# Performance work log

Hardware: AMD Instinct MI355X
Metric: run time of the kernel (lower is better)

## Reference

```python
import jax, jax.numpy as jnp
import numpy as np

D_MODEL = 1024
NUM_HEADS = 16
DEPTH = D_MODEL // NUM_HEADS  # 64
B, S = 4, 2048


def setup_inputs() -> dict:
    key = jax.random.key(0)
    ks = jax.random.split(key, 9)
    scale = 1.0 / np.sqrt(D_MODEL)
    inp = {
        "x": jax.random.normal(ks[0], (B, S, D_MODEL), dtype=jnp.float32),
        "Wq": jax.random.normal(ks[1], (D_MODEL, D_MODEL), dtype=jnp.float32) * scale,
        "bq": jnp.zeros((D_MODEL,), dtype=jnp.float32),
        "Wk": jax.random.normal(ks[2], (D_MODEL, D_MODEL), dtype=jnp.float32) * scale,
        "bk": jnp.zeros((D_MODEL,), dtype=jnp.float32),
        "Wv": jax.random.normal(ks[3], (D_MODEL, D_MODEL), dtype=jnp.float32) * scale,
        "bv": jnp.zeros((D_MODEL,), dtype=jnp.float32),
        "Wo": jax.random.normal(ks[4], (D_MODEL, D_MODEL), dtype=jnp.float32) * scale,
        "bo": jnpps if False else jnp.zeros((D_MODEL,), dtype=jnp.float32),
    }
    return inp


def reference(x, Wq, bq, Wk, bk, Wv, bv, Wo, bo):
    # q/k/v projections: [B, S, D]
    q = x @ Wq + bq
    k = x @ Wk + bk
    v = x @ Wv + bv

    def split_heads(t):  # [B, S, D] -> [B, H, S, depth]
        return t.reshape(B, S, NUM_HEADS, DEPTH).transpose(0, 2, 1, 3)

    q, k, v = split_heads(q), split_heads(k), split_heads(v)

    # scaled dot-product attention
    scores = jnp.einsum("bhqd,bhkd->bhqk", q, k) / jnp.sqrt(jnp.float32(DEPTH))
    attn = jax.nn.softmax(scores, axis=-1)  # [B, H, Sq, Sk]
    out = jnp.einsum("bhqk,bhkd->bhqd", attn, v)

    # merge heads: [B, H, S, depth] -> [B, S, D]
    out = out.transpose(0, 2, 1, 3).reshape(B, S, D_MODEL)
    return out @ Wo + bo
```

## Files before the change

kernel.cpp:

```cpp
#include <hip/hip_runtime.h>
#include <cstdint>

typedef __attribute__((ext_vector_type(8))) __bf16 bf16x8;
typedef __attribute__((ext_vector_type(4))) __bf16 bf16x4;
typedef __attribute__((ext_vector_type(4))) float f32x4;

#define S_LEN 2048
#define NH 16
#define DMODEL 1024
#define M_ROWS 8192

__device__ __forceinline__ void gload16(const void* g, void* l) {
  __builtin_amdgcn_global_load_lds(
      (const __attribute__((address_space(1))) void*)const_cast<void*>(g),
      (__attribute__((address_space(3))) void*)l, 16, 0, 0);
}

__global__ __launch_bounds__(256) void split_x_kernel(
    const float* __restrict__ in, __bf16* __restrict__ hi, __bf16* __restrict__ lo)
{
  const size_t i = ((size_t)blockIdx.x * 256 + threadIdx.x) * 4;
  const float4 v = *(const float4*)(in + i);
  const float vv[4] = {v.x, v.y, v.z, v.w};
  bf16x4 h, l;
#pragma unroll
  for (int j = 0; j < 4; ++j) {
    const __bf16 hb = (__bf16)vv[j];
    h[j] = hb;
    l[j] = (__bf16)(vv[j] - (float)hb);
  }
  *(bf16x4*)(hi + i) = h;
  *(bf16x4*)(lo + i) = l;
}

__global__ __launch_bounds__(256) void tsplit_w_kernel(
    const float* __restrict__ W, __bf16* __restrict__ th, __bf16* __restrict__ tl)
{
  __shared__ float tile[32][33];
  const int t = threadIdx.x;
  const int n0 = blockIdx.x * 32, k0 = blockIdx.y * 32;
  {
    const int r = t >> 3, c = (t & 7) * 4;
    const float4 v = *(const float4*)(W + (size_t)(k0 + r) * DMODEL + n0 + c);
    tile[r][c] = v.x; tile[r][c + 1] = v.y; tile[r][c + 2] = v.z; tile[r][c + 3] = v.w;
  }
  __syncthreads();
  const int n = t >> 3, kk = (t & 7) * 4;
  bf16x4 h, l;
#pragma unroll
  for (int j = 0; j < 4; ++j) {
    const float v = tile[kk + j][n];
    const __bf16 hb = (__bf16)v;
    h[j] = hb;
    l[j] = (__bf16)(v - (float)hb);
  }
  *(bf16x4*)(th + (size_t)(n0 + n) * DMODEL + k0 + kk) = h;
  *(bf16x4*)(tl + (size_t)(n0 + n) * DMODEL + k0 + kk) = l;
}

__global__ __launch_bounds__(256) void gemm_bf16x3_kernel(
    const __bf16* __restrict__ Ah, const __bf16* __restrict__ Al,
    const __bf16* __restrict__ Bh, const __bf16* __restrict__ Bl,
    const float* __restrict__ bias, float* __restrict__ outF,
    __bf16* __restrict__ outB, const int mode, const float scale)
{
  __shared__ __align__(16) __bf16 sAh[128 * 32];
  __shared__ __align__(16) __bf16 sAl[128 * 32];
  __shared__ __align__(16) __bf16 sBh[128 * 32];
  __shared__ __align__(16) __bf16 sBl[128 * 32];

  const int tid = threadIdx.x;
  const int w = tid >> 6, l = tid & 63;
  const int wr = w >> 1, wc = w & 1;
  const int m0 = blockIdx.x * 128, n0 = blockIdx.y * 128;
  const int q = l & 15, kg = l >> 4;

  f32x4 acc[4][4];
#pragma unroll
  for (int i = 0; i < 4; ++i)
#pragma unroll
    for (int j = 0; j < 4; ++j) acc[i][j] = f32x4{0.f, 0.f, 0.f, 0.f};

  const int sr0 = w * 32 + (l >> 2);
  const int sg = l & 3;

  for (int k0 = 0; k0 < 1024; k0 += 32) {
    __syncthreads();
#pragma unroll
    for (int u = 0; u < 2; ++u) {
      const int r = sr0 + u * 16;
      const int gs = sg ^ ((r >> 1) & 3);
      const size_t offA = (size_t)(m0 + r) * 1024 + k0 + gs * 8;
      const size_t offB = (size_t)(n0 + r) * 1024 + k0 + gs * 8;
      const int ldsoff = w * 2048 + u * 1024;
      gload16(Ah + offA, (char*)sAh + ldsoff);
      gload16(Al + offA, (char*)sAl + ldsoff);
      gload16(Bh + offB, (char*)sBh + ldsoff);
      gload16(Bl + offB, (char*)sBl + ldsoff);
    }
    __syncthreads();

    bf16x8 fah[4], fal[4], fbh[4], fbl[4];
#pragma unroll
    for (int mf = 0; mf < 4; ++mf) {
      const int row = wr * 64 + mf * 16 + q;
      const int off = row * 64 + ((kg ^ ((row >> 1) & 3)) * 16);
      fah[mf] = *(const bf16x8*)((const char*)sAh + off);
      fal[mf] = *(const bf16x8*)((const char*)sAl + off);
    }
#pragma unroll
    for (int nf = 0; nf < 4; ++nf) {
      const int n = wc * 64 + nf * 16 + q;
      const int off = n * 64 + ((kg ^ ((n >> 1) & 3)) * 16);
      fbh[nf] = *(const bf16x8*)((const char*)sBh + off);
      fbl[nf] = *(const bf16x8*)((const char*)sBl + off);
    }
#pragma unroll
    for (int mf = 0; mf < 4; ++mf)
#pragma unroll
      for (int nf = 0; nf < 4; ++nf) {
        acc[mf][nf] = __builtin_amdgcn_mfma_f32_16x16x32_bf16(fah[mf], fbh[nf], acc[mf][nf], 0, 0, 0);
        acc[mf][nf] = __builtin_amdgcn_mfma_f32_16x16x32_bf16(fah[mf], fbl[nf], acc[mf][nf], 0, 0, 0);
        acc[mf][nf] = __builtin_amdgcn_mfma_f32_16x16x32_bf16(fal[mf], fbh[nf], acc[mf][nf], 0, 0, 0);
      }
  }

#pragma unroll
  for (int mf = 0; mf < 4; ++mf) {
#pragma unroll
    for (int nf = 0; nf < 4; ++nf) {
      const int nloc = wc * 64 + nf * 16 + q;
      const int n = n0 + nloc;
      const float bv = bias[n];
      const int mbase = m0 + wr * 64 + mf * 16 + kg * 4;
      if (mode == 0) {
#pragma unroll
        for (int r = 0; r < 4; ++r)
          outF[(size_t)(mbase + r) * 1024 + n] = acc[mf][nf][r] + bv;
      } else if (mode == 1) {
#pragma unroll
        for (int r = 0; r < 4; ++r) {
          const int m = mbase + r;
          const int b = m >> 11, s = m & 2047, h = n >> 6, d = n & 63;
          outB[(((size_t)(b * NH + h)) * S_LEN + s) * 64 + d] =
              (__bf16)((acc[mf][nf][r] + bv) * scale);
        }
      } else {
        const int b = mbase >> 11, s0 = mbase & 2047, h = n >> 6, d = n & 63;
        bf16x4 pv;
#pragma unroll
        for (int r = 0; r < 4; ++r) pv[r] = (__bf16)(acc[mf][nf][r] + bv);
        *(bf16x4*)(outB + (((size_t)(b * NH + h)) * 64 + d) * S_LEN + s0) = pv;
      }
    }
  }
}

__global__ __launch_bounds__(256) void attn_mfma_kernel(
    const __bf16* __restrict__ qbuf, const __bf16* __restrict__ kbuf,
    const __bf16* __restrict__ vbufT, __bf16* __restrict__ o_hi,
    __bf16* __restrict__ o_lo)
{
  __shared__ __align__(16) __bf16 Ks[64 * 64];
  __shared__ __align__(16) __bf16 Vt[64 * 64];
  __shared__ __align__(16) __bf16 Pt[4 * 32 * 64];

  const int tid = threadIdx.x;
  const int w = tid >> 6, l = tid & 63;
  const int q = l & 15, kg = l >> 4;
  const int q7 = q & 7;
  const int bh = blockIdx.y;
  const int q0 = blockIdx.x * 128;

  bf16x8 qf[2][2];
#pragma unroll
  for (int qg = 0; qg < 2; ++qg) {
    const __bf16* qp =
        qbuf + ((size_t)bh * S_LEN + q0 + w * 32 + qg * 16 + q) * 64 + kg * 8;
    qf[qg][0] = *(const bf16x8*)qp;
    qf[qg][1] = *(const bf16x8*)(qp + 32);
  }

  float l_s[2] = {0.f, 0.f};
  f32x4 acc_o[2][4];
#pragma unroll
  for (int qg = 0; qg < 2; ++qg)
#pragma unroll
    for (int i = 0; i < 4; ++i) acc_o[qg][i] = f32x4{0.f, 0.f, 0.f, 0.f};

  char* const Pw = (char*)Pt + w * 4096;
  const int sr = w * 16 + (l >> 3);
  const int sg = l & 7;

  const int koff0 = q * 128 + ((kg ^ q7) << 4);
  const int koff1 = q * 128 + (((kg + 4) ^ q7) << 4);
  int voff[2];
#pragma unroll
  for (int kf = 0; kf < 2; ++kf) voff[kf] = ((kf * 4 + kg) ^ q7) << 4;

  for (int t = 0; t < S_LEN / 64; ++t) {
    __syncthreads();
#pragma unroll
    for (int u = 0; u < 2; ++u) {
      const int r = sr + u * 8;
      const int gs = sg ^ (r & 7);
      const int ldsoff = w * 2048 + u * 1024;
      gload16(kbuf + ((size_t)bh * S_LEN + t * 64 + r) * 64 + gs * 8, (char*)Ks + ldsoff);
      gload16(vbufT + ((size_t)bh * 64 + r) * S_LEN + t * 64 + gs * 8, (char*)Vt + ldsoff);
    }
    __syncthreads();

    f32x4 sacc[2][4];
#pragma unroll
    for (int qg = 0; qg < 2; ++qg)
#pragma unroll
      for (int mf = 0; mf < 4; ++mf) sacc[qg][mf] = f32x4{0.f, 0.f, 0.f, 0.f};

    __builtin_amdgcn_s_setprio(1);
#pragma unroll
    for (int mf = 0; mf < 4; ++mf) {
      const bf16x8 a0 = *(const bf16x8*)((const char*)Ks + mf * 2048 + koff0);
      const bf16x8 a1 = *(const bf16x8*)((const char*)Ks + mf * 2048 + koff1);
#pragma unroll
      for (int qg = 0; qg < 2; ++qg) {
        sacc[qg][mf] = __builtin_amdgcn_mfma_f32_16x16x32_bf16(a0, qf[qg][0], sacc[qg][mf], 0, 0, 0);
        sacc[qg][mf] = __builtin_amdgcn_mfma_f32_16x16x32_bf16(a1, qf[qg][1], sacc[qg][mf], 0, 0, 0);
      }
    }
    __builtin_amdgcn_s_setprio(0);

#pragma unroll
    for (int qg = 0; qg < 2; ++qg) {
      float ps = l_s[qg];
#pragma unroll
      for (int mf = 0; mf < 4; ++mf) {
        bf16x4 pv;
#pragma unroll
        for (int r = 0; r < 4; ++r) {
          const float p = exp2f(sacc[qg][mf][r]);
          ps += p;
          pv[r] = (__bf16)p;
        }
        *(bf16x4*)(Pw + (qg * 16 + q) * 128 + ((mf * 32 + kg * 8) ^ (q7 << 4))) = pv;
      }
      l_s[qg] = ps;
    }

    bf16x8 pa[2][2];
#pragma unroll
    for (int qg = 0; qg < 2; ++qg)
#pragma unroll
      for (int kf = 0; kf < 2; ++kf)
        pa[qg][kf] = *(const bf16x8*)(Pw + (qg * 16 + q) * 128 + voff[kf]);

    __builtin_amdgcn_s_setprio(1);
#pragma unroll
    for (int nf = 0; nf < 4; ++nf) {
      const bf16x8 vb0 = *(const bf16x8*)((const char*)Vt + nf * 2048 + q * 128 + voff[0]);
      const bf16x8 vb1 = *(const bf16x8*)((const char*)Vt + nf * 2048 + q * 128 + voff[1]);
#pragma unroll
      for (int qg = 0; qg < 2; ++qg) {
        acc_o[qg][nf] = __builtin_amdgcn_mfma_f32_16x16x32_bf16(pa[qg][0], vb0, acc_o[qg][nf], 0, 0, 0);
        acc_o[qg][nf] = __builtin_amdgcn_mfma_f32_16x16x32_bf16(pa[qg][1], vb1, acc_o[qg][nf], 0, 0, 0);
      }
    }
    __builtin_amdgcn_s_setprio(0);
  }

  const int b = bh >> 4, h = bh & 15;
#pragma unroll
  for (int qg = 0; qg < 2; ++qg) {
    float ps = l_s[qg];
    ps += __shfl_xor(ps, 16);
    ps += __shfl_xor(ps, 32);
    const float linv = 1.0f / ps;
    float ir[4];
#pragma unroll
    for (int r = 0; r < 4; ++r) ir[r] = __shfl(linv, (kg << 2) | r, 64);
#pragma unroll
    for (int nf = 0; nf < 4; ++nf) {
#pragma unroll
      for (int r = 0; r < 4; ++r) {
        const float val = acc_o[qg][nf][r] * ir[r];
        const __bf16 hb = (__bf16)val;
        const __bf16 lb = (__bf16)(val - (float)hb);
        const size_t row = (size_t)b * S_LEN + q0 + w * 32 + qg * 16 + (kg << 2) + r;
        const size_t col = (size_t)h * 64 + nf * 16 + q;
        o_hi[row * 1024 + col] = hb;
        o_lo[row * 1024 + col] = lb;
      }
    }
  }
}

extern "C" void kernel_launch(void* const* d_in, const int* in_sizes, int n_in,
                              void* d_out, int out_size, void* d_ws, size_t ws_size,
                              hipStream_t stream) {
  const float* x  = (const float*)d_in[0];
  const float* Wq = (const float*)d_in[1];
  const float* bq = (const float*)d_in[2];
  const float* Wk = (const float*)d_in[3];
  const float* bk = (const float*)d_in[4];
  const float* Wv = (const float*)d_in[5];
  const float* bv = (const float*)d_in[6];
  const float* Wo = (const float*)d_in[7];
  const float* bo = (const float*)d_in[8];
  float* out = (float*)d_out;

  char* ws = (char*)d_ws;
  const size_t XB = 16777216ull;
  __bf16* x_hi  = (__bf16*)(ws);
  __bf16* x_lo  = (__bf16*)(ws + XB);
  __bf16* qbuf  = (__bf16*)(ws + 2 * XB);
  __bf16* kbuf  = (__bf16*)(ws + 3 * XB);
  __bf16* vbufT = (__bf16*)(ws + 4 * XB);
  __bf16* wt    = (__bf16*)(ws + 5 * XB);
  const size_t WE = 1048576ull;
  __bf16* wtq_h = wt + 0 * WE; __bf16* wtq_l = wt + 1 * WE;
  __bf16* wtk_h = wt + 2 * WE; __bf16* wtk_l = wt + 3 * WE;
  __bf16* wtv_h = wt + 4 * WE; __bf16* wtv_l = wt + 5 * WE;
  __bf16* wto_h = wt + 6 * WE; __bf16* wto_l = wt + 7 * WE;

  split_x_kernel<<<8192, 256, 0, stream>>>(x, x_hi, x_lo);
  tsplit_w_kernel<<<dim3(32, 32), 256, 0, stream>>>(Wq, wtq_h, wtq_l);
  tsplit_w_kernel<<<dim3(32, 32), 256, 0, stream>>>(Wk, wtk_h, wtk_l);
  tsplit_w_kernel<<<dim3(32, 32), 256, 0, stream>>>(Wv, wtv_h, wtv_l);
  tsplit_w_kernel<<<dim3(32, 32), 256, 0, stream>>>(Wo, wto_h, wto_l);

  const dim3 gg(64, 8);
  gemm_bf16x3_kernel<<<gg, 256, 0, stream>>>(x_hi, x_lo, wtq_h, wtq_l, bq,
                                             nullptr, qbuf, 1, 0.18033688011112042f);
  gemm_bf16x3_kernel<<<gg, 256, 0, stream>>>(x_hi, x_lo, wtk_h, wtk_l, bk,
                                             nullptr, kbuf, 1, 1.0f);
  gemm_bf16x3_kernel<<<gg, 256, 0, stream>>>(x_hi, x_lo, wtv_h, wtv_l, bv,
                                             nullptr, vbufT, 2, 1.0f);
  attn_mfma_kernel<<<dim3(16, 64), 256, 0, stream>>>(qbuf, kbuf, vbufT, x_hi, x_lo);
  gemm_bf16x3_kernel<<<gg, 256, 0, stream>>>(x_hi, x_lo, wto_h, wto_l, bo,
                                             out, nullptr, 0, 1.0f);
}
```

Before: 438.0 us.

## Double-buffer K/V tiles in attention kernel to overlap loads with MFMA compute

Allocates two LDS buffers for the K and V tiles and restructures the key loop so the next tile's global-to-LDS loads are issued before computing on the current tile. This removes one of the two barriers per iteration and hides load latency behind the score and PV matrix multiplies. It doubles K/V LDS usage, which may lower occupancy. Correctness depends on global_load_lds completion being covered by the single remaining barrier per tile.

Result: no change. 445.1 us (+1.6%).

```diff
diff --git a/kernel.cpp b/kernel.cpp
--- a/kernel.cpp
+++ b/kernel.cpp
@@ -161,8 +161,8 @@
     const __bf16* __restrict__ vbufT, __bf16* __restrict__ o_hi,
     __bf16* __restrict__ o_lo)
 {
-  __shared__ __align__(16) __bf16 Ks[64 * 64];
-  __shared__ __align__(16) __bf16 Vt[64 * 64];
+  __shared__ __align__(16) __bf16 Ks[2][64 * 64];
+  __shared__ __align__(16) __bf16 Vt[2][64 * 64];
   __shared__ __align__(16) __bf16 Pt[4 * 32 * 64];
 
   const int tid = threadIdx.x;
@@ -198,18 +198,20 @@
 #pragma unroll
   for (int kf = 0; kf < 2; ++kf) voff[kf] = ((kf * 4 + kg) ^ q7) << 4;
 
-  for (int t = 0; t < S_LEN / 64; ++t) {
-    __syncthreads();
+  auto STAGE = [&](int buf, int t) {
 #pragma unroll
     for (int u = 0; u < 2; ++u) {
       const int r = sr + u * 8;
       const int gs = sg ^ (r & 7);
       const int ldsoff = w * 2048 + u * 1024;
-      gload16(kbuf + ((size_t)bh * S_LEN + t * 64 + r) * 64 + gs * 8, (char*)Ks + ldsoff);
-      gload16(vbufT + ((size_t)bh * 64 + r) * S_LEN + t * 64 + gs * 8, (char*)Vt + ldsoff);
-    }
-    __syncthreads();
-
+      gload16(kbuf + ((size_t)bh * S_LEN + t * 64 + r) * 64 + gs * 8,
+              (char*)Ks[buf] + ldsoff);
+      gload16(vbufT + ((size_t)bh * 64 + r) * S_LEN + t * 64 + gs * 8,
+              (char*)Vt[buf] + ldsoff);
+    }
+  };
+
+  auto COMPUTE = [&](const __bf16* Ksb, const __bf16* Vtb) {
     f32x4 sacc[2][4];
 #pragma unroll
     for (int qg = 0; qg < 2; ++qg)
@@ -219,8 +221,8 @@
     __builtin_amdgcn_s_setprio(1);
 #pragma unroll
     for (int mf = 0; mf < 4; ++mf) {
-      const bf16x8 a0 = *(const bf16x8*)((const char*)Ks + mf * 2048 + koff0);
-      const bf16x8 a1 = *(const bf16x8*)((const char*)Ks + mf * 2048 + koff1);
+      const bf16x8 a0 = *(const bf16x8*)((const char*)Ksb + mf * 2048 + koff0);
+      const bf16x8 a1 = *(const bf16x8*)((const char*)Ksb + mf * 2048 + koff1);
 #pragma unroll
       for (int qg = 0; qg < 2; ++qg) {
         sacc[qg][mf] = __builtin_amdgcn_mfma_f32_16x16x32_bf16(a0, qf[qg][0], sacc[qg][mf], 0, 0, 0);
@@ -256,8 +258,8 @@
     __builtin_amdgcn_s_setprio(1);
 #pragma unroll
     for (int nf = 0; nf < 4; ++nf) {
-      const bf16x8 vb0 = *(const bf16x8*)((const char*)Vt + nf * 2048 + q * 128 + voff[0]);
-      const bf16x8 vb1 = *(const bf16x8*)((const char*)Vt + nf * 2048 + q * 128 + voff[1]);
+      const bf16x8 vb0 = *(const bf16x8*)((const char*)Vtb + nf * 2048 + q * 128 + voff[0]);
+      const bf16x8 vb1 = *(const bf16x8*)((const char*)Vtb + nf * 2048 + q * 128 + voff[1]);
 #pragma unroll
       for (int qg = 0; qg < 2; ++qg) {
         acc_o[qg][nf] = __builtin_amdgcn_mfma_f32_16x16x32_bf16(pa[qg][0], vb0, acc_o[qg][nf], 0, 0, 0);
@@ -265,6 +267,19 @@
       }
     }
     __builtin_amdgcn_s_setprio(0);
+  };
+
+  STAGE(0, 0);
+  __syncthreads();
+
+  for (int t = 0; t < S_LEN / 64; t += 2) {
+    STAGE(1, t + 1);
+    COMPUTE(Ks[0], Vt[0]);
+    __syncthreads();
+
+    if (t + 2 < S_LEN / 64) STAGE(0, t + 2);
+    COMPUTE(Ks[1], Vt[1]);
+    __syncthreads();
   }
 
   const int b = bh >> 4, h = bh & 15;
```
